# Optimization experiments

Measured on AMD Instinct MI355X. Metric: run time of the kernel, lower is better.

Reference implementation:

```python
import jax, jax.numpy as jnp
import numpy as np

N = 8000          # num_nodes
DEG = 8           # avg out-degree of random road graph
B = 32            # batch size
INPUT_DIM = 2
UNITS = 64        # rnn_units
K = 2             # max_diffusion_step
NUM_SUPPORTS = 2  # dual_random_walk


def _spmm(rows, cols, vals, x):
    # sparse @ dense: y[r] += vals * x[c] for each coo entry (r, c)
    return jax.ops.segment_sum(vals[:, None] * x[cols], rows, num_segments=N)


def _gconv(inputs, state, supports, W, b):
    # Chebyshev-style diffusion conv, faithful to GCONV.forward layout
    Bsz = inputs.shape[0]
    x = jnp.concatenate([inputs.reshape(Bsz, N, -1), state.reshape(Bsz, N, -1)], axis=2)
    F = x.shape[2]                                   # input_dim + units
    x0 = jnp.transpose(x, (1, 2, 0)).reshape(N, F * Bsz)
    xs = [x0]
    for rows, cols, vals in supports:
        x1 = _spmm(rows, cols, vals, x0)
        xs.append(x1)
        xk2, xk1 = x0, x1
        for _ in range(2, K + 1):
            x2 = 2.0 * _spmm(rows, cols, vals, xk1) - xk2
            xs.append(x2)
            xk2, xk1 = xk1, x2
    M = len(xs)                                      # num_matrices = 2*K+1
    xc = jnp.stack(xs).reshape(M, N, F, Bsz)
    xc = jnp.transpose(xc, (3, 1, 2, 0)).reshape(Bsz * N, F * M)
    out = xc @ W + b
    return out.reshape(Bsz, N * W.shape[1])


def setup_inputs() -> dict:
    rng = np.random.default_rng(0)
    rows = np.repeat(np.arange(N, dtype=np.int32), DEG)
    cols = rng.integers(0, N, size=N * DEG).astype(np.int32)
    vals = rng.uniform(0.5, 1.5, size=N * DEG).astype(np.float32)
    # random-walk normalization: rw(A) = D^-1 A ; supports are rw(A).T and rw(A.T).T
    rsum = np.zeros(N, np.float32); np.add.at(rsum, rows, vals)
    csum = np.zeros(N, np.float32); np.add.at(csum, cols, vals)
    rinv = np.where(rsum > 0, 1.0 / np.maximum(rsum, 1e-12), 0.0).astype(np.float32)
    cinv = np.where(csum > 0, 1.0 / np.maximum(csum, 1e-12), 0.0).astype(np.float32)
    # support0 = (D^-1 A)^T: entry (cols[i], rows[i]) = vals[i] * rinv[rows[i]]
    s0_rows, s0_cols, s0_vals = cols, rows, (vals * rinv[rows]).astype(np.float32)
    # support1 = (D_T^-1 A^T)^T: entry (rows[i], cols[i]) = vals[i] * cinv[cols[i]]
    s1_rows, s1_cols, s1_vals = rows, cols, (vals * cinv[cols]).astype(np.float32)

    key = jax.random.key(0)
    k1, k2, k3, k4 = jax.random.split(key, 4)
    F = INPUT_DIM + UNITS
    M = NUM_SUPPORTS * K + 1
    xavier = lambda k, shape: jax.random.normal(k, shape, jnp.float32) * np.float32(np.sqrt(2.0 / (shape[0] + shape[1])))
    W_ru = xavier(k1, (F * M, 2 * UNITS))
    b_ru = jnp.ones((2 * UNITS,), jnp.float32)    # bias_start=1.0
    W_c = xavier(k2, (F * M, UNITS))
    b_c = jnp.zeros((UNITS,), jnp.float32)        # bias_start=0.0
    inputs = jax.random.normal(k3, (B, N * INPUT_DIM), jnp.float32)
    hx = jax.random.normal(k4, (B, N * UNITS), jnp.float32)
    return {
        "inputs": inputs, "hx": hx,
        "W_ru": W_ru, "b_ru": b_ru, "W_c": W_c, "b_c": b_c,
        "s0_rows": jnp.asarray(s0_rows), "s0_cols": jnp.asarray(s0_cols), "s0_vals": jnp.asarray(s0_vals),
        "s1_rows": jnp.asarray(s1_rows), "s1_cols": jnp.asarray(s1_cols), "s1_vals": jnp.asarray(s1_vals),
    }


def reference(inputs, hx, W_ru, b_ru, W_c, b_c,
              s0_rows, s0_cols, s0_vals, s1_rows, s1_cols, s1_vals):
    supports = [(s0_rows, s0_cols, s0_vals), (s1_rows, s1_cols, s1_vals)]
    value = jax.nn.sigmoid(_gconv(inputs, hx, supports, W_ru, b_ru))
    value = value.reshape(-1, N, 2 * UNITS)
    r = value[..., :UNITS].reshape(-1, N * UNITS)
    u = value[..., UNITS:].reshape(-1, N * UNITS)
    c = jnp.tanh(_gconv(inputs, r * hx, supports, W_c, b_c))
    return u * hx + (1.0 - u) * c
```

## Files before the change

### kernel.cpp

```cpp
#include <hip/hip_runtime.h>
#include <stdint.h>

typedef unsigned short u16;
typedef unsigned int   u32;

typedef __attribute__((ext_vector_type(8))) short bf16x8;
typedef __attribute__((ext_vector_type(4))) float f32x4;

#define NNODES 8000
#define BSZ    32
#define UNITS  64
#define EDG    64000
#define ROWCH  288
#define ROWU16 2304
#define KLIN   480
#define HXROW  512000
#define INROW  16000
#define NROW   18432000

__device__ __forceinline__ u32 f2bf(float f){
    u32 u = __float_as_uint(f);
    return (u + 0x7FFFu + ((u >> 16) & 1u)) >> 16;
}
__device__ __forceinline__ float bfu(u16 s){ return __uint_as_float(((u32)s) << 16); }
__device__ __forceinline__ float lo16(u32 u){ return __uint_as_float(u << 16); }
__device__ __forceinline__ float hi16(u32 u){ return __uint_as_float(u & 0xFFFF0000u); }
__device__ __forceinline__ float sigm(float x){ return 1.f / (1.f + __expf(-x)); }

__global__ void hist_k(const int* __restrict__ rows, int* __restrict__ counts){
    int e = blockIdx.x * 256 + threadIdx.x;
    if (e < EDG) atomicAdd(&counts[rows[e]], 1);
}

__global__ __launch_bounds__(256) void scan_k(const int* __restrict__ counts,
                                              int* __restrict__ row_ptr,
                                              int* __restrict__ cursor){
    __shared__ int part[256];
    int t = threadIdx.x;
    int s = 0;
    for (int i = 0; i < 32; ++i){ int r = t*32 + i; if (r < NNODES) s += counts[r]; }
    part[t] = s;
    __syncthreads();
    if (t == 0){
        int run = 0;
        for (int i = 0; i < 256; ++i){ int v = part[i]; part[i] = run; run += v; }
    }
    __syncthreads();
    int run = part[t];
    for (int i = 0; i < 32; ++i){
        int r = t*32 + i;
        if (r < NNODES){ row_ptr[r] = run; cursor[r] = run; run += counts[r]; }
    }
    if (t == 255) row_ptr[NNODES] = run;
}

__global__ void scatter_k(const int* __restrict__ rows, const int* __restrict__ cols,
                          const float* __restrict__ vals, int* __restrict__ cursor,
                          int* __restrict__ cs, float* __restrict__ vs){
    int e = blockIdx.x * 256 + threadIdx.x;
    if (e < EDG){
        int r = rows[e];
        int slot = atomicAdd(&cursor[r], 1);
        cs[slot] = cols[e];
        vs[slot] = vals[e];
    }
}

__global__ void prep_w_k(const float* __restrict__ W_ru, const float* __restrict__ W_c,
                         u16* __restrict__ Wt_ru, u16* __restrict__ Wt_c){
    int id = blockIdx.x * 256 + threadIdx.x;
    if (id < 128*KLIN){
        int c = id / KLIN, kl = id % KLIN;
        int m = kl / 96, fp = kl - m*96;
        u16 v = 0;
        if (fp < 66) v = (u16)f2bf(W_ru[(fp*5 + m)*128 + c]);
        Wt_ru[id] = v;
    }
    int id2 = id - 128*KLIN;
    if (id2 >= 0 && id2 < 64*KLIN){
        int c = id2 / KLIN, kl = id2 % KLIN;
        int m = kl / 96, fp = kl - m*96;
        u16 v = 0;
        if (fp < 66) v = (u16)f2bf(W_c[(fp*5 + m)*64 + c]);
        Wt_c[id2] = v;
    }
}

__global__ __launch_bounds__(256) void build_x0_k(const float* __restrict__ inputs,
                                                  const float* __restrict__ hx,
                                                  u16* __restrict__ X0){
    __shared__ float sl[32*72];
    int n = blockIdx.x, t = threadIdx.x;
    #pragma unroll
    for (int i = 0; i < 8; ++i){
        int idx = t + i*256;
        int b = idx >> 6, f = idx & 63;
        sl[b*72 + 2 + f] = hx[b*HXROW + n*64 + f];
    }
    if (t < 64){
        int b = t >> 1, d = t & 1;
        sl[b*72 + d] = inputs[b*INROW + n*2 + d];
    }
    if (t < 192){
        int b = t / 6, k = t - b*6;
        sl[b*72 + 66 + k] = 0.f;
    }
    __syncthreads();
    #pragma unroll
    for (int i = 0; i < 2; ++i){
        int j = t + i*256;
        if (j < ROWCH){
            int b = j & 31, s = j >> 5;
            const float* p = &sl[b*72 + s*8];
            uint4 o;
            o.x = f2bf(p[0]) | (f2bf(p[1]) << 16);
            o.y = f2bf(p[2]) | (f2bf(p[3]) << 16);
            o.z = f2bf(p[4]) | (f2bf(p[5]) << 16);
            o.w = f2bf(p[6]) | (f2bf(p[7]) << 16);
            ((uint4*)X0)[n*ROWCH + j] = o;
        }
    }
}

__device__ __forceinline__ void acc8(float* a, uint4 q, float v){
    a[0] += v*lo16(q.x); a[1] += v*hi16(q.x);
    a[2] += v*lo16(q.y); a[3] += v*hi16(q.y);
    a[4] += v*lo16(q.z); a[5] += v*hi16(q.z);
    a[6] += v*lo16(q.w); a[7] += v*hi16(q.w);
}
__device__ __forceinline__ uint4 pack8(const float* a){
    uint4 o;
    o.x = f2bf(a[0]) | (f2bf(a[1]) << 16);
    o.y = f2bf(a[2]) | (f2bf(a[3]) << 16);
    o.z = f2bf(a[4]) | (f2bf(a[5]) << 16);
    o.w = f2bf(a[6]) | (f2bf(a[7]) << 16);
    return o;
}

__global__ __launch_bounds__(288) void diff1_k(const u16* __restrict__ X0,
                                               u16* __restrict__ X1a, u16* __restrict__ X1b,
                                               const int* __restrict__ rp,
                                               const int* __restrict__ c0, const float* __restrict__ v0,
                                               const int* __restrict__ c1, const float* __restrict__ v1){
    int t = threadIdx.x;
    if (t >= ROWCH) return;
    int n = blockIdx.x;
    const uint4* xb = (const uint4*)X0;
    float a[8] = {0,0,0,0,0,0,0,0};
    float d[8] = {0,0,0,0,0,0,0,0};
    {
        uint4 q[8]; float vv[8];
        #pragma unroll
        for (int i = 0; i < 8; ++i){
            int c = c1[n*8 + i]; vv[i] = v1[n*8 + i];
            q[i] = xb[(size_t)c*ROWCH + t];
        }
        #pragma unroll
        for (int i = 0; i < 8; ++i) acc8(d, q[i], vv[i]);
    }
    int e = rp[n], end = rp[n+1];
    for (; e + 8 <= end; e += 8){
        uint4 q[8]; float vv[8];
        #pragma unroll
        for (int i = 0; i < 8; ++i){
            int c = c0[e+i]; vv[i] = v0[e+i];
            q[i] = xb[(size_t)c*ROWCH + t];
        }
        #pragma unroll
        for (int i = 0; i < 8; ++i) acc8(a, q[i], vv[i]);
    }
    for (; e < end; ++e){
        int c = c0[e]; float v = v0[e];
        acc8(a, xb[(size_t)c*ROWCH + t], v);
    }
    ((uint4*)X1a)[(size_t)n*ROWCH + t] = pack8(a);
    ((uint4*)X1b)[(size_t)n*ROWCH + t] = pack8(d);
}

__global__ __launch_bounds__(288) void diff2_k(const u16* __restrict__ X0,
                                               const u16* __restrict__ X1a, const u16* __restrict__ X1b,
                                               u16* __restrict__ X2a, u16* __restrict__ X2b,
                                               const int* __restrict__ rp,
                                               const int* __restrict__ c0, const float* __restrict__ v0,
                                               const int* __restrict__ c1, const float* __restrict__ v1){
    int t = threadIdx.x;
    if (t >= ROWCH) return;
    int n = blockIdx.x;
    const uint4* xa = (const uint4*)X1a;
    const uint4* xbb = (const uint4*)X1b;
    uint4 pv = ((const uint4*)X0)[(size_t)n*ROWCH + t];
    float a[8] = {0,0,0,0,0,0,0,0};
    float d[8] = {0,0,0,0,0,0,0,0};
    {
        uint4 q[8]; float vv[8];
        #pragma unroll
        for (int i = 0; i < 8; ++i){
            int c = c1[n*8 + i]; vv[i] = v1[n*8 + i];
            q[i] = xbb[(size_t)c*ROWCH + t];
        }
        #pragma unroll
        for (int i = 0; i < 8; ++i) acc8(d, q[i], vv[i]);
    }
    int e = rp[n], end = rp[n+1];
    for (; e + 8 <= end; e += 8){
        uint4 q[8]; float vv[8];
        #pragma unroll
        for (int i = 0; i < 8; ++i){
            int c = c0[e+i]; vv[i] = v0[e+i];
            q[i] = xa[(size_t)c*ROWCH + t];
        }
        #pragma unroll
        for (int i = 0; i < 8; ++i) acc8(a, q[i], vv[i]);
    }
    for (; e < end; ++e){
        int c = c0[e]; float v = v0[e];
        acc8(a, xa[(size_t)c*ROWCH + t], v);
    }
    float p[8] = { lo16(pv.x), hi16(pv.x), lo16(pv.y), hi16(pv.y),
                   lo16(pv.z), hi16(pv.z), lo16(pv.w), hi16(pv.w) };
    #pragma unroll
    for (int i = 0; i < 8; ++i){ a[i] = 2.f*a[i] - p[i]; d[i] = 2.f*d[i] - p[i]; }
    ((uint4*)X2a)[(size_t)n*ROWCH + t] = pack8(a);
    ((uint4*)X2b)[(size_t)n*ROWCH + t] = pack8(d);
}

__global__ __launch_bounds__(256) void gemm_ru_k(
        const u16* X0, const u16* __restrict__ X1a, const u16* __restrict__ X2a,
        const u16* __restrict__ X1b, const u16* __restrict__ X2b,
        const u16* __restrict__ Wt,
        const float* __restrict__ b_ru,
        u16* __restrict__ U, u16* X0st){
    const int t = threadIdx.x;
    const int lane = t & 63, w = t >> 6;
    const int node = blockIdx.x*4 + w;
    const int cIn = lane & 15, q = lane >> 4;
    const size_t noff = (size_t)node * ROWU16;

    const u16* xp[5] = { X0 + noff, X1a + noff, X2a + noff, X1b + noff, X2b + noff };

    f32x4 acc[2][8];
    const f32x4 z4 = {0.f,0.f,0.f,0.f};
    #pragma unroll
    for (int rt = 0; rt < 2; ++rt)
        #pragma unroll
        for (int ct = 0; ct < 8; ++ct) acc[rt][ct] = z4;

    bf16x8 ca0, ca1, cb[8], na0, na1, nb[8];
    ca0 = *(const bf16x8*)&xp[0][(size_t)((0*4 + q)*32 + 0*16 + cIn)*8];
    ca1 = *(const bf16x8*)&xp[0][(size_t)((0*4 + q)*32 + 1*16 + cIn)*8];
    #pragma unroll
    for (int ct = 0; ct < 8; ++ct)
        cb[ct] = *(const bf16x8*)&Wt[(ct*16 + cIn)*KLIN + 0*32 + q*8];

    #pragma unroll
    for (int st = 0; st < 15; ++st){
        if (st < 14){
            const int m2 = (st+1)/3, sub2 = (st+1) - m2*3;
            na0 = *(const bf16x8*)&xp[m2][(size_t)((sub2*4 + q)*32 + 0*16 + cIn)*8];
            na1 = *(const bf16x8*)&xp[m2][(size_t)((sub2*4 + q)*32 + 1*16 + cIn)*8];
            #pragma unroll
            for (int ct = 0; ct < 8; ++ct)
                nb[ct] = *(const bf16x8*)&Wt[(ct*16 + cIn)*KLIN + (st+1)*32 + q*8];
        }
        #pragma unroll
        for (int ct = 0; ct < 8; ++ct){
            acc[0][ct] = __builtin_amdgcn_mfma_f32_16x16x32_bf16(ca0, cb[ct], acc[0][ct], 0,0,0);
            acc[1][ct] = __builtin_amdgcn_mfma_f32_16x16x32_bf16(ca1, cb[ct], acc[1][ct], 0,0,0);
        }
        ca0 = na0; ca1 = na1;
        #pragma unroll
        for (int ct = 0; ct < 8; ++ct) cb[ct] = nb[ct];
    }

    #pragma unroll
    for (int ct = 0; ct < 8; ++ct){
        int col = ct*16 + cIn;
        float bias = b_ru[col];
        #pragma unroll
        for (int rt = 0; rt < 2; ++rt){
            int b0 = rt*16 + q*4;
            f32x4 d = acc[rt][ct];
            if (ct < 4){
                int fp = 2 + col;
                int s = fp >> 3, off = fp & 7;
                #pragma unroll
                for (int i = 0; i < 4; ++i){
                    size_t idx = noff + (size_t)(s*32 + b0 + i)*8 + off;
                    float h = bfu(X0st[idx]);
                    float rg = sigm(d[i] + bias);
                    X0st[idx] = (u16)f2bf(rg * h);
                }
            } else {
                uint2 pk;
                float v0 = sigm(d[0] + bias), v1 = sigm(d[1] + bias);
                float v2 = sigm(d[2] + bias), v3 = sigm(d[3] + bias);
                pk.x = f2bf(v0) | (f2bf(v1) << 16);
                pk.y = f2bf(v2) | (f2bf(v3) << 16);
                *(uint2*)&U[(size_t)node*2048 + (col - 64)*32 + b0] = pk;
            }
        }
    }
}

__global__ __launch_bounds__(256) void gemm_c_k(
        const u16* __restrict__ X0, const u16* __restrict__ X1a, const u16* __restrict__ X2a,
        const u16* __restrict__ X1b, const u16* __restrict__ X2b,
        const u16* __restrict__ Wt,
        const float* __restrict__ b_c, const float* __restrict__ hx,
        const u16* __restrict__ U, float* __restrict__ out){
    const int t = threadIdx.x;
    const int lane = t & 63, w = t >> 6;
    const int node = blockIdx.x*4 + w;
    const int cIn = lane & 15, q = lane >> 4;
    const size_t noff = (size_t)node * ROWU16;

    const u16* xp[5] = { X0 + noff, X1a + noff, X2a + noff, X1b + noff, X2b + noff };

    f32x4 acc[2][4];
    const f32x4 z4 = {0.f,0.f,0.f,0.f};
    #pragma unroll
    for (int rt = 0; rt < 2; ++rt)
        #pragma unroll
        for (int ct = 0; ct < 4; ++ct) acc[rt][ct] = z4;

    bf16x8 ca0, ca1, cb[4], na0, na1, nb[4];
    ca0 = *(const bf16x8*)&xp[0][(size_t)((0*4 + q)*32 + 0*16 + cIn)*8];
    ca1 = *(const bf16x8*)&xp[0][(size_t)((0*4 + q)*32 + 1*16 + cIn)*8];
    #pragma unroll
    for (int ct = 0; ct < 4; ++ct)
        cb[ct] = *(const bf16x8*)&Wt[(ct*16 + cIn)*KLIN + 0*32 + q*8];

    #pragma unroll
    for (int st = 0; st < 15; ++st){
        if (st < 14){
            const int m2 = (st+1)/3, sub2 = (st+1) - m2*3;
            na0 = *(const bf16x8*)&xp[m2][(size_t)((sub2*4 + q)*32 + 0*16 + cIn)*8];
            na1 = *(const bf16x8*)&xp[m2][(size_t)((sub2*4 + q)*32 + 1*16 + cIn)*8];
            #pragma unroll
            for (int ct = 0; ct < 4; ++ct)
                nb[ct] = *(const bf16x8*)&Wt[(ct*16 + cIn)*KLIN + (st+1)*32 + q*8];
        }
        #pragma unroll
        for (int ct = 0; ct < 4; ++ct){
            acc[0][ct] = __builtin_amdgcn_mfma_f32_16x16x32_bf16(ca0, cb[ct], acc[0][ct], 0,0,0);
            acc[1][ct] = __builtin_amdgcn_mfma_f32_16x16x32_bf16(ca1, cb[ct], acc[1][ct], 0,0,0);
        }
        ca0 = na0; ca1 = na1;
        #pragma unroll
        for (int ct = 0; ct < 4; ++ct) cb[ct] = nb[ct];
    }

    #pragma unroll
    for (int ct = 0; ct < 4; ++ct){
        int col = ct*16 + cIn;
        float bias = b_c[col];
        #pragma unroll
        for (int rt = 0; rt < 2; ++rt){
            int b0 = rt*16 + q*4;
            f32x4 d = acc[rt][ct];
            uint2 up = *(const uint2*)&U[(size_t)node*2048 + col*32 + b0];
            float uu[4] = { lo16(up.x), hi16(up.x), lo16(up.y), hi16(up.y) };
            #pragma unroll
            for (int i = 0; i < 4; ++i){
                float c = tanhf(d[i] + bias);
                size_t gi = (size_t)(b0 + i)*HXROW + node*64 + col;
                float h = hx[gi];
                out[gi] = uu[i]*h + (1.f - uu[i])*c;
            }
        }
    }
}

extern "C" void kernel_launch(void* const* d_in, const int* in_sizes, int n_in,
                              void* d_out, int out_size, void* d_ws, size_t ws_size,
                              hipStream_t stream){
    const float* inputs = (const float*)d_in[0];
    const float* hx     = (const float*)d_in[1];
    const float* W_ru   = (const float*)d_in[2];
    const float* b_ru   = (const float*)d_in[3];
    const float* W_c    = (const float*)d_in[4];
    const float* b_c    = (const float*)d_in[5];
    const int*   s0r    = (const int*)d_in[6];
    const int*   s0c    = (const int*)d_in[7];
    const float* s0v    = (const float*)d_in[8];
    const int*   s1c    = (const int*)d_in[10];
    const float* s1v    = (const float*)d_in[11];
    float* out = (float*)d_out;

    char* ws = (char*)d_ws;
    size_t off = 0;
    auto alloc = [&](size_t bytes) -> char* {
        char* p = ws + off;
        off += (bytes + 255) & ~(size_t)255;
        return p;
    };
    const size_t XBYTES = (size_t)NROW*2 + 2048;
    u16* X0   = (u16*)alloc(XBYTES);
    u16* X1a  = (u16*)alloc(XBYTES);
    u16* X2a  = (u16*)alloc(XBYTES);
    u16* X1b  = (u16*)alloc(XBYTES);
    u16* X2b  = (u16*)alloc(XBYTES);
    u16* U    = (u16*)alloc((size_t)NNODES*2048*2);
    u16* WtRU = (u16*)alloc((size_t)128*KLIN*2);
    u16* WtC  = (u16*)alloc((size_t)64*KLIN*2);
    int* counts  = (int*)alloc((size_t)NNODES*4);
    int* row_ptr = (int*)alloc((size_t)(NNODES+1)*4);
    int* cursor  = (int*)alloc((size_t)NNODES*4);
    int*   cols_s = (int*)alloc((size_t)EDG*4);
    float* vals_s = (float*)alloc((size_t)EDG*4);
    (void)ws_size; (void)in_sizes; (void)n_in; (void)out_size;

    hipMemsetAsync(counts, 0, (size_t)NNODES*4, stream);
    hist_k<<<250, 256, 0, stream>>>(s0r, counts);
    scan_k<<<1, 256, 0, stream>>>(counts, row_ptr, cursor);
    scatter_k<<<250, 256, 0, stream>>>(s0r, s0c, s0v, cursor, cols_s, vals_s);

    prep_w_k<<<360, 256, 0, stream>>>(W_ru, W_c, WtRU, WtC);
    build_x0_k<<<NNODES, 256, 0, stream>>>(inputs, hx, X0);

    diff1_k<<<NNODES, 288, 0, stream>>>(X0, X1a, X1b, row_ptr, cols_s, vals_s, s1c, s1v);
    diff2_k<<<NNODES, 288, 0, stream>>>(X0, X1a, X1b, X2a, X2b, row_ptr, cols_s, vals_s, s1c, s1v);

    gemm_ru_k<<<NNODES/4, 256, 0, stream>>>(X0, X1a, X2a, X1b, X2b, WtRU, b_ru, U, X0);

    diff1_k<<<NNODES, 288, 0, stream>>>(X0, X1a, X1b, row_ptr, cols_s, vals_s, s1c, s1v);
    diff2_k<<<NNODES, 288, 0, stream>>>(X0, X1a, X1b, X2a, X2b, row_ptr, cols_s, vals_s, s1c, s1v);

    gemm_c_k<<<NNODES/4, 256, 0, stream>>>(X0, X1a, X2a, X1b, X2b, WtC, b_c, hx, U, out);
}
```

Measured before the change: 722.1 us.

## Interleave diffusion matrices per node and stage GEMM A-tiles through LDS

All five diffusion matrices now live in one per-node row of 12 slices of 72 features, padded and zeroed, replacing five separate buffers. The diffusion step becomes one kernel that handles both supports via block index and processes two chunks per thread. The GEMMs process 8 nodes per block and double-buffer A tiles into LDS with global_load_lds, cutting K padding from 480 to 384. The aim is better GEMM locality and less padding work, at the cost of strided gathers and heavier LDS use.

```diff
diff --git a/kernel.cpp b/kernel.cpp
--- a/kernel.cpp
+++ b/kernel.cpp
@@ -8,15 +8,13 @@
 typedef __attribute__((ext_vector_type(4))) float f32x4;
 
 #define NNODES 8000
-#define BSZ    32
-#define UNITS  64
 #define EDG    64000
-#define ROWCH  288
-#define ROWU16 2304
-#define KLIN   480
+#define KLIN   384
+#define NCHK   1536
+#define ROWB   24576
+#define ROWU16 12288
 #define HXROW  512000
 #define INROW  16000
-#define NROW   18432000
 
 __device__ __forceinline__ u32 f2bf(float f){
     u32 u = __float_as_uint(f);
@@ -70,25 +68,25 @@
                          u16* __restrict__ Wt_ru, u16* __restrict__ Wt_c){
     int id = blockIdx.x * 256 + threadIdx.x;
     if (id < 128*KLIN){
-        int c = id / KLIN, kl = id % KLIN;
-        int m = kl / 96, fp = kl - m*96;
+        int c = id / KLIN, kl = id - c*KLIN;
+        int m = kl / 72, f = kl - m*72;
         u16 v = 0;
-        if (fp < 66) v = (u16)f2bf(W_ru[(fp*5 + m)*128 + c]);
+        if (m < 5 && f < 66) v = (u16)f2bf(W_ru[(f*5 + m)*128 + c]);
         Wt_ru[id] = v;
     }
     int id2 = id - 128*KLIN;
     if (id2 >= 0 && id2 < 64*KLIN){
-        int c = id2 / KLIN, kl = id2 % KLIN;
-        int m = kl / 96, fp = kl - m*96;
+        int c = id2 / KLIN, kl = id2 - c*KLIN;
+        int m = kl / 72, f = kl - m*72;
         u16 v = 0;
-        if (fp < 66) v = (u16)f2bf(W_c[(fp*5 + m)*64 + c]);
+        if (m < 5 && f < 66) v = (u16)f2bf(W_c[(f*5 + m)*64 + c]);
         Wt_c[id2] = v;
     }
 }
 
 __global__ __launch_bounds__(256) void build_x0_k(const float* __restrict__ inputs,
                                                   const float* __restrict__ hx,
-                                                  u16* __restrict__ X0){
+                                                  u16* __restrict__ X){
     __shared__ float sl[32*72];
     int n = blockIdx.x, t = threadIdx.x;
     #pragma unroll
@@ -106,10 +104,11 @@
         sl[b*72 + 66 + k] = 0.f;
     }
     __syncthreads();
+    uint4* xr = (uint4*)(X + (size_t)n*ROWU16);
     #pragma unroll
     for (int i = 0; i < 2; ++i){
         int j = t + i*256;
-        if (j < ROWCH){
+        if (j < 288){
             int b = j & 31, s = j >> 5;
             const float* p = &sl[b*72 + s*8];
             uint4 o;
@@ -117,8 +116,12 @@
             o.y = f2bf(p[2]) | (f2bf(p[3]) << 16);
             o.z = f2bf(p[4]) | (f2bf(p[5]) << 16);
             o.w = f2bf(p[6]) | (f2bf(p[7]) << 16);
-            ((uint4*)X0)[n*ROWCH + j] = o;
-        }
+            xr[j] = o;
+        }
+    }
+    if (t < 96){
+        uint4 z; z.x = z.y = z.z = z.w = 0;
+        xr[1440 + t] = z;
     }
 }
 
@@ -137,160 +140,152 @@
     return o;
 }
 
-__global__ __launch_bounds__(288) void diff1_k(const u16* __restrict__ X0,
-                                               u16* __restrict__ X1a, u16* __restrict__ X1b,
-                                               const int* __restrict__ rp,
-                                               const int* __restrict__ c0, const float* __restrict__ v0,
-                                               const int* __restrict__ c1, const float* __restrict__ v1){
-    int t = threadIdx.x;
-    if (t >= ROWCH) return;
-    int n = blockIdx.x;
-    const uint4* xb = (const uint4*)X0;
-    float a[8] = {0,0,0,0,0,0,0,0};
-    float d[8] = {0,0,0,0,0,0,0,0};
-    {
-        uint4 q[8]; float vv[8];
+__global__ __launch_bounds__(256) void diff_k(u16* X,
+                                              const int* __restrict__ rp,
+                                              const int* __restrict__ c0, const float* __restrict__ v0,
+                                              const int* __restrict__ c1, const float* __restrict__ v1,
+                                              int srcA, int dstA, int srcB, int dstB, int lvl2){
+    int blk = blockIdx.x;
+    int matB = (blk >= 4500) ? 1 : 0;
+    int id = (blk - matB*4500)*256 + threadIdx.x;
+    int n = id / 144;
+    int rr = id - n*144;
+    int s = rr >> 4, bp = rr & 15;
+    int src = matB ? srcB : srcA;
+    int dst = matB ? dstB : dstA;
+    const int* cc; const float* vv; int start, end;
+    if (matB){ cc = c1; vv = v1; start = n*8; end = start + 8; }
+    else     { cc = c0; vv = v0; start = rp[n]; end = rp[n+1]; }
+
+    const uint4* xb = (const uint4*)X;
+    int co0 = (src + s)*32 + bp;
+    int co1 = co0 + 16;
+
+    float a0[8] = {0,0,0,0,0,0,0,0};
+    float a1[8] = {0,0,0,0,0,0,0,0};
+    int e = start;
+    for (; e + 8 <= end; e += 8){
+        uint4 qa[8], qb[8]; float wv[8];
         #pragma unroll
         for (int i = 0; i < 8; ++i){
-            int c = c1[n*8 + i]; vv[i] = v1[n*8 + i];
-            q[i] = xb[(size_t)c*ROWCH + t];
-        }
-        #pragma unroll
-        for (int i = 0; i < 8; ++i) acc8(d, q[i], vv[i]);
-    }
-    int e = rp[n], end = rp[n+1];
-    for (; e + 8 <= end; e += 8){
-        uint4 q[8]; float vv[8];
-        #pragma unroll
-        for (int i = 0; i < 8; ++i){
-            int c = c0[e+i]; vv[i] = v0[e+i];
-            q[i] = xb[(size_t)c*ROWCH + t];
-        }
-        #pragma unroll
-        for (int i = 0; i < 8; ++i) acc8(a, q[i], vv[i]);
+            int c = cc[e+i]; wv[i] = vv[e+i];
+            size_t rb = (size_t)c*NCHK;
+            qa[i] = xb[rb + co0];
+            qb[i] = xb[rb + co1];
+        }
+        #pragma unroll
+        for (int i = 0; i < 8; ++i){ acc8(a0, qa[i], wv[i]); acc8(a1, qb[i], wv[i]); }
     }
     for (; e < end; ++e){
-        int c = c0[e]; float v = v0[e];
-        acc8(a, xb[(size_t)c*ROWCH + t], v);
-    }
-    ((uint4*)X1a)[(size_t)n*ROWCH + t] = pack8(a);
-    ((uint4*)X1b)[(size_t)n*ROWCH + t] = pack8(d);
-}
-
-__global__ __launch_bounds__(288) void diff2_k(const u16* __restrict__ X0,
-                                               const u16* __restrict__ X1a, const u16* __restrict__ X1b,
-                                               u16* __restrict__ X2a, u16* __restrict__ X2b,
-                                               const int* __restrict__ rp,
-                                               const int* __restrict__ c0, const float* __restrict__ v0,
-                                               const int* __restrict__ c1, const float* __restrict__ v1){
-    int t = threadIdx.x;
-    if (t >= ROWCH) return;
-    int n = blockIdx.x;
-    const uint4* xa = (const uint4*)X1a;
-    const uint4* xbb = (const uint4*)X1b;
-    uint4 pv = ((const uint4*)X0)[(size_t)n*ROWCH + t];
-    float a[8] = {0,0,0,0,0,0,0,0};
-    float d[8] = {0,0,0,0,0,0,0,0};
-    {
-        uint4 q[8]; float vv[8];
-        #pragma unroll
-        for (int i = 0; i < 8; ++i){
-            int c = c1[n*8 + i]; vv[i] = v1[n*8 + i];
-            q[i] = xbb[(size_t)c*ROWCH + t];
-        }
-        #pragma unroll
-        for (int i = 0; i < 8; ++i) acc8(d, q[i], vv[i]);
-    }
-    int e = rp[n], end = rp[n+1];
-    for (; e + 8 <= end; e += 8){
-        uint4 q[8]; float vv[8];
-        #pragma unroll
-        for (int i = 0; i < 8; ++i){
-            int c = c0[e+i]; vv[i] = v0[e+i];
-            q[i] = xa[(size_t)c*ROWCH + t];
-        }
-        #pragma unroll
-        for (int i = 0; i < 8; ++i) acc8(a, q[i], vv[i]);
-    }
-    for (; e < end; ++e){
-        int c = c0[e]; float v = v0[e];
-        acc8(a, xa[(size_t)c*ROWCH + t], v);
-    }
-    float p[8] = { lo16(pv.x), hi16(pv.x), lo16(pv.y), hi16(pv.y),
-                   lo16(pv.z), hi16(pv.z), lo16(pv.w), hi16(pv.w) };
-    #pragma unroll
-    for (int i = 0; i < 8; ++i){ a[i] = 2.f*a[i] - p[i]; d[i] = 2.f*d[i] - p[i]; }
-    ((uint4*)X2a)[(size_t)n*ROWCH + t] = pack8(a);
-    ((uint4*)X2b)[(size_t)n*ROWCH + t] = pack8(d);
-}
-
-__global__ __launch_bounds__(256) void gemm_ru_k(
-        const u16* X0, const u16* __restrict__ X1a, const u16* __restrict__ X2a,
-        const u16* __restrict__ X1b, const u16* __restrict__ X2b,
-        const u16* __restrict__ Wt,
-        const float* __restrict__ b_ru,
-        u16* __restrict__ U, u16* X0st){
+        int c = cc[e]; float v = vv[e];
+        size_t rb = (size_t)c*NCHK;
+        acc8(a0, xb[rb + co0], v);
+        acc8(a1, xb[rb + co1], v);
+    }
+    if (lvl2){
+        uint4 p0 = xb[(size_t)n*NCHK + s*32 + bp];
+        uint4 p1 = xb[(size_t)n*NCHK + s*32 + bp + 16];
+        float pa[8] = { lo16(p0.x), hi16(p0.x), lo16(p0.y), hi16(p0.y),
+                        lo16(p0.z), hi16(p0.z), lo16(p0.w), hi16(p0.w) };
+        float pb[8] = { lo16(p1.x), hi16(p1.x), lo16(p1.y), hi16(p1.y),
+                        lo16(p1.z), hi16(p1.z), lo16(p1.w), hi16(p1.w) };
+        #pragma unroll
+        for (int i = 0; i < 8; ++i){ a0[i] = 2.f*a0[i] - pa[i]; a1[i] = 2.f*a1[i] - pb[i]; }
+    }
+    uint4* yb = (uint4*)X;
+    yb[(size_t)n*NCHK + (dst + s)*32 + bp]      = pack8(a0);
+    yb[(size_t)n*NCHK + (dst + s)*32 + bp + 16] = pack8(a1);
+}
+
+__device__ __forceinline__ void stage_step(const char* xbase, int j, char* lbase, int t){
+    int w = t >> 6, lane = t & 63;
+    #pragma unroll
+    for (int i = 0; i < 4; ++i){
+        int p = w*4 + i;
+        int nd = p >> 1, h = p & 1;
+        const char* g = xbase + nd*ROWB + j*2048 + h*1024 + lane*16;
+        char* l = lbase + nd*2048 + h*1024 + lane*16;
+        __builtin_amdgcn_global_load_lds(
+            (const __attribute__((address_space(1))) u32*)g,
+            (__attribute__((address_space(3))) u32*)l, 16, 0, 0);
+    }
+}
+
+__global__ __launch_bounds__(256, 2) void gemm_ru_k(
+        u16* X, const u16* __restrict__ Wt, const float* __restrict__ b_ru,
+        u16* __restrict__ U){
+    __shared__ u16 sA[18432];
     const int t = threadIdx.x;
     const int lane = t & 63, w = t >> 6;
-    const int node = blockIdx.x*4 + w;
     const int cIn = lane & 15, q = lane >> 4;
-    const size_t noff = (size_t)node * ROWU16;
-
-    const u16* xp[5] = { X0 + noff, X1a + noff, X2a + noff, X1b + noff, X2b + noff };
-
-    f32x4 acc[2][8];
+    const int node0 = blockIdx.x * 8;
+    const char* xbase = (const char*)X + (size_t)node0*ROWB;
+
+    f32x4 acc[4][8];
     const f32x4 z4 = {0.f,0.f,0.f,0.f};
     #pragma unroll
-    for (int rt = 0; rt < 2; ++rt)
+    for (int rt = 0; rt < 4; ++rt)
         #pragma unroll
         for (int ct = 0; ct < 8; ++ct) acc[rt][ct] = z4;
 
-    bf16x8 ca0, ca1, cb[8], na0, na1, nb[8];
-    ca0 = *(const bf16x8*)&xp[0][(size_t)((0*4 + q)*32 + 0*16 + cIn)*8];
-    ca1 = *(const bf16x8*)&xp[0][(size_t)((0*4 + q)*32 + 1*16 + cIn)*8];
+    bf16x8 cb[8], nb[8];
+    stage_step(xbase, 0, (char*)sA, t);
     #pragma unroll
     for (int ct = 0; ct < 8; ++ct)
-        cb[ct] = *(const bf16x8*)&Wt[(ct*16 + cIn)*KLIN + 0*32 + q*8];
-
-    #pragma unroll
-    for (int st = 0; st < 15; ++st){
-        if (st < 14){
-            const int m2 = (st+1)/3, sub2 = (st+1) - m2*3;
-            na0 = *(const bf16x8*)&xp[m2][(size_t)((sub2*4 + q)*32 + 0*16 + cIn)*8];
-            na1 = *(const bf16x8*)&xp[m2][(size_t)((sub2*4 + q)*32 + 1*16 + cIn)*8];
+        cb[ct] = *(const bf16x8*)&Wt[(ct*16 + cIn)*KLIN + q*8];
+    __syncthreads();
+
+    for (int j = 0; j < 12; ++j){
+        const int cur = j & 1;
+        if (j < 11){
+            stage_step(xbase, j+1, (char*)sA + (cur^1)*16384, t);
             #pragma unroll
             for (int ct = 0; ct < 8; ++ct)
-                nb[ct] = *(const bf16x8*)&Wt[(ct*16 + cIn)*KLIN + (st+1)*32 + q*8];
-        }
-        #pragma unroll
-        for (int ct = 0; ct < 8; ++ct){
-            acc[0][ct] = __builtin_amdgcn_mfma_f32_16x16x32_bf16(ca0, cb[ct], acc[0][ct], 0,0,0);
-            acc[1][ct] = __builtin_amdgcn_mfma_f32_16x16x32_bf16(ca1, cb[ct], acc[1][ct], 0,0,0);
-        }
-        ca0 = na0; ca1 = na1;
+                nb[ct] = *(const bf16x8*)&Wt[(ct*16 + cIn)*KLIN + (j+1)*32 + q*8];
+        }
+        const u16* As = sA + cur*8192;
+        #pragma unroll
+        for (int rt = 0; rt < 4; ++rt){
+            int nd = w*2 + (rt >> 1);
+            int b  = (rt & 1)*16 + cIn;
+            bf16x8 a = *(const bf16x8*)&As[nd*1024 + (q*32 + b)*8];
+            #pragma unroll
+            for (int ct = 0; ct < 8; ++ct)
+                acc[rt][ct] = __builtin_amdgcn_mfma_f32_16x16x32_bf16(a, cb[ct], acc[rt][ct], 0,0,0);
+        }
         #pragma unroll
         for (int ct = 0; ct < 8; ++ct) cb[ct] = nb[ct];
-    }
-
+        __syncthreads();
+    }
+
+    uint4* eL = (uint4*)sA;
+    #pragma unroll
+    for (int i = 0; i < 9; ++i){
+        int idx = t + i*256;
+        int nd = idx / 288, c = idx - nd*288;
+        eL[idx] = *(const uint4*)(xbase + (size_t)nd*ROWB + c*16);
+    }
+    __syncthreads();
     #pragma unroll
     for (int ct = 0; ct < 8; ++ct){
         int col = ct*16 + cIn;
         float bias = b_ru[col];
         #pragma unroll
-        for (int rt = 0; rt < 2; ++rt){
-            int b0 = rt*16 + q*4;
+        for (int rt = 0; rt < 4; ++rt){
+            int nd = w*2 + (rt >> 1);
+            int b0 = (rt & 1)*16 + q*4;
             f32x4 d = acc[rt][ct];
             if (ct < 4){
-                int fp = 2 + col;
+                int fp = col + 2;
                 int s = fp >> 3, off = fp & 7;
                 #pragma unroll
                 for (int i = 0; i < 4; ++i){
-                    size_t idx = noff + (size_t)(s*32 + b0 + i)*8 + off;
-                    float h = bfu(X0st[idx]);
-                    float rg = sigm(d[i] + bias);
-                    X0st[idx] = (u16)f2bf(rg * h);
+                    int li = (nd*288 + s*32 + b0 + i)*8 + off;
+                    float h = bfu(sA[li]);
+                    sA[li] = (u16)f2bf(sigm(d[i] + bias) * h);
                 }
             } else {
+                int node = node0 + nd;
                 uint2 pk;
                 float v0 = sigm(d[0] + bias), v1 = sigm(d[1] + bias);
                 float v2 = sigm(d[2] + bias), v3 = sigm(d[3] + bias);
@@ -300,54 +295,60 @@
             }
         }
     }
-}
-
-__global__ __launch_bounds__(256) void gemm_c_k(
-        const u16* __restrict__ X0, const u16* __restrict__ X1a, const u16* __restrict__ X2a,
-        const u16* __restrict__ X1b, const u16* __restrict__ X2b,
-        const u16* __restrict__ Wt,
-        const float* __restrict__ b_c, const float* __restrict__ hx,
-        const u16* __restrict__ U, float* __restrict__ out){
+    __syncthreads();
+    #pragma unroll
+    for (int i = 0; i < 9; ++i){
+        int idx = t + i*256;
+        int nd = idx / 288, c = idx - nd*288;
+        *(uint4*)((char*)X + (size_t)(node0 + nd)*ROWB + c*16) = eL[idx];
+    }
+}
+
+__global__ __launch_bounds__(256, 2) void gemm_c_k(
+        const u16* __restrict__ X, const u16* __restrict__ Wt, const float* __restrict__ b_c,
+        const float* __restrict__ hx, const u16* __restrict__ U, float* __restrict__ out){
+    __shared__ u16 sA[16384];
     const int t = threadIdx.x;
     const int lane = t & 63, w = t >> 6;
-    const int node = blockIdx.x*4 + w;
     const int cIn = lane & 15, q = lane >> 4;
-    const size_t noff = (size_t)node * ROWU16;
-
-    const u16* xp[5] = { X0 + noff, X1a + noff, X2a + noff, X1b + noff, X2b + noff };
-
-    f32x4 acc[2][4];
+    const int node0 = blockIdx.x * 8;
+    const char* xbase = (const char*)X + (size_t)node0*ROWB;
+
+    f32x4 acc[4][4];
     const f32x4 z4 = {0.f,0.f,0.f,0.f};
     #pragma unroll
-    for (int rt = 0; rt < 2; ++rt)
+    for (int rt = 0; rt < 4; ++rt)
         #pragma unroll
         for (int ct = 0; ct < 4; ++ct) acc[rt][ct] = z4;
 
-    bf16x8 ca0, ca1, cb[4], na0, na1, nb[4];
-    ca0 = *(const bf16x8*)&xp[0][(size_t)((0*4 + q)*32 + 0*16 + cIn)*8];
-    ca1 = *(const bf16x8*)&xp[0][(size_t)((0*4 + q)*32 + 1*16 + cIn)*8];
+    bf16x8 cb[4], nb[4];
+    stage_step(xbase, 0, (char*)sA, t);
     #pragma unroll
     for (int ct = 0; ct < 4; ++ct)
-        cb[ct] = *(const bf16x8*)&Wt[(ct*16 + cIn)*KLIN + 0*32 + q*8];
-
-    #pragma unroll
-    for (int st = 0; st < 15; ++st){
-        if (st < 14){
-            const int m2 = (st+1)/3, sub2 = (st+1) - m2*3;
-            na0 = *(const bf16x8*)&xp[m2][(size_t)((sub2*4 + q)*32 + 0*16 + cIn)*8];
-            na1 = *(const bf16x8*)&xp[m2][(size_t)((sub2*4 + q)*32 + 1*16 + cIn)*8];
+        cb[ct] = *(const bf16x8*)&Wt[(ct*16 + cIn)*KLIN + q*8];
+    __syncthreads();
+
+    for (int j = 0; j < 12; ++j){
+        const int cur = j & 1;
+        if (j < 11){
+            stage_step(xbase, j+1, (char*)sA + (cur^1)*16384, t);
             #pragma unroll
             for (int ct = 0; ct < 4; ++ct)
-                nb[ct] = *(const bf16x8*)&Wt[(ct*16 + cIn)*KLIN + (st+1)*32 + q*8];
-        }
-        #pragma unroll
-        for (int ct = 0; ct < 4; ++ct){
-            acc[0][ct] = __builtin_amdgcn_mfma_f32_16x16x32_bf16(ca0, cb[ct], acc[0][ct], 0,0,0);
-            acc[1][ct] = __builtin_amdgcn_mfma_f32_16x16x32_bf16(ca1, cb[ct], acc[1][ct], 0,0,0);
-        }
-        ca0 = na0; ca1 = na1;
+                nb[ct] = *(const bf16x8*)&Wt[(ct*16 + cIn)*KLIN + (j+1)*32 + q*8];
+        }
+        const u16* As = sA + cur*8192;
+        #pragma unroll
+        for (int rt = 0; rt < 4; ++rt){
+            int nd = w*2 + (rt >> 1);
+            int b  = (rt & 1)*16 + cIn;
+            bf16x8 a = *(const bf16x8*)&As[nd*1024 + (q*32 + b)*8];
+            #pragma unroll
+            for (int ct = 0; ct < 4; ++ct)
+                acc[rt][ct] = __builtin_amdgcn_mfma_f32_16x16x32_bf16(a, cb[ct], acc[rt][ct], 0,0,0);
+        }
         #pragma unroll
         for (int ct = 0; ct < 4; ++ct) cb[ct] = nb[ct];
+        __syncthreads();
     }
 
     #pragma unroll
@@ -355,15 +356,17 @@
         int col = ct*16 + cIn;
         float bias = b_c[col];
         #pragma unroll
-        for (int rt = 0; rt < 2; ++rt){
-            int b0 = rt*16 + q*4;
+        for (int rt = 0; rt < 4; ++rt){
+            int nd = w*2 + (rt >> 1);
+            int b0 = (rt & 1)*16 + q*4;
+            int node = node0 + nd;
             f32x4 d = acc[rt][ct];
             uint2 up = *(const uint2*)&U[(size_t)node*2048 + col*32 + b0];
             float uu[4] = { lo16(up.x), hi16(up.x), lo16(up.y), hi16(up.y) };
             #pragma unroll
             for (int i = 0; i < 4; ++i){
                 float c = tanhf(d[i] + bias);
-                size_t gi = (size_t)(b0 + i)*HXROW + node*64 + col;
+                size_t gi = (size_t)(b0 + i)*HXROW + (size_t)node*64 + col;
                 float h = hx[gi];
                 out[gi] = uu[i]*h + (1.f - uu[i])*c;
             }
@@ -394,12 +397,7 @@
         off += (bytes + 255) & ~(size_t)255;
         return p;
     };
-    const size_t XBYTES = (size_t)NROW*2 + 2048;
-    u16* X0   = (u16*)alloc(XBYTES);
-    u16* X1a  = (u16*)alloc(XBYTES);
-    u16* X2a  = (u16*)alloc(XBYTES);
-    u16* X1b  = (u16*)alloc(XBYTES);
-    u16* X2b  = (u16*)alloc(XBYTES);
+    u16* X    = (u16*)alloc((size_t)NNODES*ROWB);
     u16* U    = (u16*)alloc((size_t)NNODES*2048*2);
     u16* WtRU = (u16*)alloc((size_t)128*KLIN*2);
     u16* WtC  = (u16*)alloc((size_t)64*KLIN*2);
@@ -415,16 +413,16 @@
     scan_k<<<1, 256, 0, stream>>>(counts, row_ptr, cursor);
     scatter_k<<<250, 256, 0, stream>>>(s0r, s0c, s0v, cursor, cols_s, vals_s);
 
-    prep_w_k<<<360, 256, 0, stream>>>(W_ru, W_c, WtRU, WtC);
-    build_x0_k<<<NNODES, 256, 0, stream>>>(inputs, hx, X0);
-
-    diff1_k<<<NNODES, 288, 0, stream>>>(X0, X1a, X1b, row_ptr, cols_s, vals_s, s1c, s1v);
-    diff2_k<<<NNODES, 288, 0, stream>>>(X0, X1a, X1b, X2a, X2b, row_ptr, cols_s, vals_s, s1c, s1v);
-
-    gemm_ru_k<<<NNODES/4, 256, 0, stream>>>(X0, X1a, X2a, X1b, X2b, WtRU, b_ru, U, X0);
-
-    diff1_k<<<NNODES, 288, 0, stream>>>(X0, X1a, X1b, row_ptr, cols_s, vals_s, s1c, s1v);
-    diff2_k<<<NNODES, 288, 0, stream>>>(X0, X1a, X1b, X2a, X2b, row_ptr, cols_s, vals_s, s1c, s1v);
-
-    gemm_c_k<<<NNODES/4, 256, 0, stream>>>(X0, X1a, X2a, X1b, X2b, WtC, b_c, hx, U, out);
-}
+    prep_w_k<<<288, 256, 0, stream>>>(W_ru, W_c, WtRU, WtC);
+    build_x0_k<<<NNODES, 256, 0, stream>>>(inputs, hx, X);
+
+    diff_k<<<9000, 256, 0, stream>>>(X, row_ptr, cols_s, vals_s, s1c, s1v, 0, 9, 0, 27, 0);
+    diff_k<<<9000, 256, 0, stream>>>(X, row_ptr, cols_s, vals_s, s1c, s1v, 9, 18, 27, 36, 1);
+
+    gemm_ru_k<<<NNODES/8, 256, 0, stream>>>(X, WtRU, b_ru, U);
+
+    diff_k<<<9000, 256, 0, stream>>>(X, row_ptr, cols_s, vals_s, s1c, s1v, 0, 9, 0, 27, 0);
+    diff_k<<<9000, 256, 0, stream>>>(X, row_ptr, cols_s, vals_s, s1c, s1v, 9, 18, 27, 36, 1);
+
+    gemm_c_k<<<NNODES/8, 256, 0, stream>>>(X, WtC, b_c, hx, U, out);
+}
```

After: 724.0 us. Within noise of the previous version (+0.3%).
